# Kernel tuning notes

Measured on AMD Instinct MI355X. Metric: run time of the kernel, lower is better.

## Reference

```python
import jax, jax.numpy as jnp
import numpy as np

B, N, M, C, H = 8, 1024, 128, 1024, 16
D = C // H
MLP = int(C * 4.0)
EPS = 1e-6


def setup_inputs() -> dict:
    key = jax.random.key(0)
    ks = jax.random.split(key, 24)
    def w(k, shape):
        return jax.random.normal(k, shape, jnp.float32) * 0.02
    mask = jax.random.randint(ks[3], (B, M), 0, 2, dtype=jnp.int32)
    mask = mask.at[:, 0].set(1)  # ensure at least one attendable token per row
    return {
        "x": jax.random.normal(ks[0], (B, N, C), jnp.float32),
        "c_dino": jax.random.normal(ks[1], (B, C), jnp.float32),
        "c_text": jax.random.normal(ks[2], (B, M, C), jnp.float32),
        "text_mask": mask,
        "W_ada": w(ks[4], (C, 6 * C)), "b_ada": jnp.zeros((6 * C,), jnp.float32),
        "W_qkv": w(ks[5], (C, 3 * C)), "b_qkv": jnp.zeros((3 * C,), jnp.float32),
        "W_proj_sa": w(ks[6], (C, C)), "b_proj_sa": jnp.zeros((C,), jnp.float32),
        "W_q": w(ks[7], (C, C)), "b_q": jnp.zeros((C,), jnp.float32),
        "W_kv": w(ks[8], (C, 2 * C)), "b_kv": jnp.zeros((2 * C,), jnp.float32),
        "W_proj_ca": w(ks[9], (C, C)), "b_proj_ca": jnp.zeros((C,), jnp.float32),
        "W_fc1": w(ks[10], (C, MLP)), "b_fc1": jnp.zeros((MLP,), jnp.float32),
        "W_fc2": w(ks[11], (MLP, C)), "b_fc2": jnp.zeros((C,), jnp.float32),
    }


def _ln(x):
    # LayerNorm without affine params, eps=1e-6
    mu = jnp.mean(x, axis=-1, keepdims=True)
    xc = x - mu
    var = jnp.mean(xc * xc, axis=-1, keepdims=True)
    return xc * jax.lax.rsqrt(var + EPS)


def _modulate(x, shift, scale):
    return x * (1.0 + scale[:, None, :]) + shift[:, None, :]


def _heads(t):
    b, n, _ = t.shape
    return t.reshape(b, n, H, D)


def reference(x, c_dino, c_text, text_mask,
              W_ada, b_ada, W_qkv, b_qkv, W_proj_sa, b_proj_sa,
              W_q, b_q, W_kv, b_kv, W_proj_ca, b_proj_ca,
              W_fc1, b_fc1, W_fc2, b_fc2):
    scale = D ** (-0.5)
    ada = jax.nn.silu(c_dino) @ W_ada + b_ada  # (B, 6C)
    sh_msa, sc_msa, sh_ca, sc_ca, sh_mlp, sc_mlp = jnp.split(ada, 6, axis=1)

    # --- self-attention ---
    h = _modulate(_ln(x), sh_msa, sc_msa)
    qkv = h @ W_qkv + b_qkv
    q, k, v = (_heads(t) for t in jnp.split(qkv, 3, axis=-1))  # (B,N,H,D)
    attn = jax.nn.softmax(jnp.einsum('bnhd,bmhd->bhnm', q, k) * scale, axis=-1)
    sa = jnp.einsum('bhnm,bmhd->bnhd', attn, v).reshape(B, N, C) @ W_proj_sa + b_proj_sa
    x = x + sa

    # --- cross-attention ---
    h = _modulate(_ln(x), sh_ca, sc_ca)
    q = _heads(h @ W_q + b_q)                 # (B,N,H,D)
    kv = c_text @ W_kv + b_kv
    k, v = (_heads(t) for t in jnp.split(kv, 2, axis=-1))  # (B,M,H,D)
    scores = jnp.einsum('bnhd,bmhd->bhnm', q, k) * scale
    scores = jnp.where(text_mask[:, None, None, :] == 0, -jnp.inf, scores)
    attn = jax.nn.softmax(scores, axis=-1)
    ca = jnp.einsum('bhnm,bmhd->bnhd', attn, v).reshape(B, N, C) @ W_proj_ca + b_proj_ca
    x = x + ca

    # --- MLP ---
    h = _modulate(_ln(x), sh_mlp, sc_mlp)
    mlp = jax.nn.gelu(h @ W_fc1 + b_fc1, approximate=True) @ W_fc2 + b_fc2
    return x + mlp
```

## Files before the change

### kernel.cpp

```cpp
#include <hip/hip_runtime.h>
#include <hip/hip_bf16.h>

#define B_   8
#define N_   1024
#define M_   128
#define C_   1024
#define H_   16
#define D_   64
#define MLP_ 4096

typedef __bf16 bf16;
typedef __bf16 bf16x8 __attribute__((ext_vector_type(8)));
typedef __bf16 bf16x4 __attribute__((ext_vector_type(4)));
typedef float  f32x4  __attribute__((ext_vector_type(4)));

__device__ __forceinline__ f32x4 mfma16(bf16x8 a, bf16x8 b, f32x4 c) {
    return __builtin_amdgcn_mfma_f32_16x16x32_bf16(a, b, c, 0, 0, 0);
}

__device__ __forceinline__ void gload16(const bf16* g, bf16* l) {
    __builtin_amdgcn_global_load_lds(
        (const __attribute__((address_space(1))) void*)g,
        (__attribute__((address_space(3))) void*)l, 16, 0, 0);
}

__global__ __launch_bounds__(256) void transpose_k(const float* __restrict__ W,
                                                   bf16* __restrict__ Wt,
                                                   int K, int Nc) {
    __shared__ float tile[32][33];
    const int x  = threadIdx.x & 31;
    const int y0 = threadIdx.x >> 5;
    const size_t n0 = (size_t)blockIdx.x * 32;
    const size_t k0 = (size_t)blockIdx.y * 32;
#pragma unroll
    for (int i = 0; i < 4; i++)
        tile[y0 + i * 8][x] = W[(k0 + y0 + i * 8) * Nc + n0 + x];
    __syncthreads();
#pragma unroll
    for (int i = 0; i < 4; i++)
        Wt[(n0 + y0 + i * 8) * K + k0 + x] = (bf16)tile[x][y0 + i * 8];
}

__global__ __launch_bounds__(256) void vtrans_k(const bf16* __restrict__ in, int instride,
                                                int coff, int Mk, bf16* __restrict__ outT) {
    __shared__ bf16 t[32][33];
    const int tx = threadIdx.x & 31;
    const int ty0 = threadIdx.x >> 5;
    const int m0  = blockIdx.x * 32;
    const int hd0 = blockIdx.y * 32;
    const int b   = blockIdx.z;
#pragma unroll
    for (int i = 0; i < 4; i++)
        t[ty0 + i * 8][tx] = in[((size_t)(b * Mk + m0 + ty0 + i * 8)) * instride + coff + hd0 + tx];
    __syncthreads();
#pragma unroll
    for (int i = 0; i < 4; i++)
        outT[((size_t)(b * 1024 + hd0 + ty0 + i * 8)) * Mk + m0 + tx] = t[tx][ty0 + i * 8];
}

__global__ __launch_bounds__(256) void cvt_bf16_k(const float* __restrict__ in,
                                                  bf16* __restrict__ out, int n4) {
    int i = blockIdx.x * 256 + threadIdx.x;
    if (i < n4) {
        float4 v = ((const float4*)in)[i];
        bf16x4 o;
        o[0] = (bf16)v.x; o[1] = (bf16)v.y; o[2] = (bf16)v.z; o[3] = (bf16)v.w;
        ((bf16x4*)out)[i] = o;
    }
}

__global__ __launch_bounds__(256) void ada_init_k(const float* __restrict__ bias,
                                                  float* __restrict__ ada) {
    int i = blockIdx.x * 256 + threadIdx.x;
    ada[i] = bias[i % 6144];
}

__global__ __launch_bounds__(256) void ada_k(const float* __restrict__ cdino,
                                             const float* __restrict__ W,
                                             float* __restrict__ ada) {
    __shared__ float sc[8][32];
    const int tid = threadIdx.x;
    const int k0  = blockIdx.y * 32;
    {
        float c = cdino[(tid >> 5) * 1024 + k0 + (tid & 31)];
        sc[tid >> 5][tid & 31] = c / (1.f + __expf(-c));
    }
    __syncthreads();
    const int col = blockIdx.x * 256 + tid;
    float acc[8];
#pragma unroll
    for (int b = 0; b < 8; b++) acc[b] = 0.f;
    for (int kk = 0; kk < 32; kk++) {
        float w = W[(size_t)(k0 + kk) * 6144 + col];
#pragma unroll
        for (int b = 0; b < 8; b++) acc[b] += sc[b][kk] * w;
    }
#pragma unroll
    for (int b = 0; b < 8; b++) atomicAdd(&ada[(size_t)b * 6144 + col], acc[b]);
}

__global__ __launch_bounds__(256) void ln_mod_k(const float* __restrict__ X,
                                                const float* __restrict__ ada,
                                                int shoff, int scoff,
                                                bf16* __restrict__ Hout) {
    const int row = blockIdx.x;
    const int b   = row >> 10;
    const int tid = threadIdx.x;
    const float4 v = ((const float4*)(X + (size_t)row * C_))[tid];
    float s  = v.x + v.y + v.z + v.w;
    float sq = v.x * v.x + v.y * v.y + v.z * v.z + v.w * v.w;
#pragma unroll
    for (int off = 32; off; off >>= 1) {
        s  += __shfl_xor(s,  off);
        sq += __shfl_xor(sq, off);
    }
    __shared__ float rs_[4], rq_[4];
    if ((tid & 63) == 0) { rs_[tid >> 6] = s; rq_[tid >> 6] = sq; }
    __syncthreads();
    s  = rs_[0] + rs_[1] + rs_[2] + rs_[3];
    sq = rq_[0] + rq_[1] + rq_[2] + rq_[3];
    const float mu   = s * (1.f / 1024.f);
    const float var  = sq * (1.f / 1024.f) - mu * mu;
    const float rstd = rsqrtf(var + 1e-6f);
    const float4 scv = ((const float4*)(ada + (size_t)b * 6144 + scoff))[tid];
    const float4 shv = ((const float4*)(ada + (size_t)b * 6144 + shoff))[tid];
    bf16x4 o;
    o[0] = (bf16)(((v.x - mu) * rstd) * (1.f + scv.x) + shv.x);
    o[1] = (bf16)(((v.y - mu) * rstd) * (1.f + scv.y) + shv.y);
    o[2] = (bf16)(((v.z - mu) * rstd) * (1.f + scv.z) + shv.z);
    o[3] = (bf16)(((v.w - mu) * rstd) * (1.f + scv.w) + shv.w);
    *(bf16x4*)(Hout + (size_t)row * C_ + tid * 4) = o;
}

template <int MODE>
__global__ __launch_bounds__(512, 2) void gemm256w_k(const bf16* __restrict__ A,
                                                     const bf16* __restrict__ Bt,
                                                     const float* __restrict__ bias,
                                                     bf16* __restrict__ outB,
                                                     int Ncols, int K, int GX) {
    __shared__ __attribute__((aligned(16))) bf16 As[4][256][32];
    __shared__ __attribute__((aligned(16))) bf16 Bs[4][256][32];

    const int tid  = threadIdx.x;
    const int lane = tid & 63, wave = tid >> 6;
    const int lrow = lane & 15, quad = lane >> 4;
    const int wm = wave >> 2, wn = wave & 3;

    const unsigned lid = blockIdx.x;
    const unsigned cpx = gridDim.x >> 3;
    const unsigned g   = (lid & 7) * cpx + (lid >> 3);
    const size_t bm = (size_t)(g / GX) * 256;
    const size_t bn = (size_t)(g % GX) * 256;

    const int r0 = tid >> 2;
    const int cs = ((tid & 3) ^ ((r0 >> 1) & 3)) * 8;
    const bf16* gA0 = A  + (bm + r0) * (size_t)K + cs;
    const bf16* gA1 = gA0 + (size_t)128 * K;
    const bf16* gB0 = Bt + (bn + r0) * (size_t)K + cs;
    const bf16* gB1 = gB0 + (size_t)128 * K;

    f32x4 acc[8][4];
#pragma unroll
    for (int i = 0; i < 8; i++)
#pragma unroll
        for (int j = 0; j < 4; j++) acc[i][j] = (f32x4){0.f, 0.f, 0.f, 0.f};

    auto stage = [&](int bb, int koff) {
        bf16* la = &As[bb][0][0] + wave * 512;
        gload16(gA0 + koff, la);
        gload16(gA1 + koff, la + 4096);
        bf16* lb = &Bs[bb][0][0] + wave * 512;
        gload16(gB0 + koff, lb);
        gload16(gB1 + koff, lb + 4096);
    };

    const int xo = (quad ^ ((lrow >> 1) & 3)) * 8;

    bf16x8 bq[4], af[4];
    auto readB = [&](int bb) {
        const bf16(*Bp)[32] = Bs[bb];
#pragma unroll
        for (int ni = 0; ni < 4; ni++)
            bq[ni] = *(const bf16x8*)&Bp[wn * 64 + ni * 16 + lrow][xo];
    };
    auto readA4 = [&](int bb, int h) {
        const bf16(*Ap)[32] = As[bb];
#pragma unroll
        for (int mi = 0; mi < 4; mi++)
            af[mi] = *(const bf16x8*)&Ap[wm * 128 + h * 64 + mi * 16 + lrow][xo];
    };
    auto mfmac = [&](int h) {
        __builtin_amdgcn_s_setprio(1);
#pragma unroll
        for (int mi = 0; mi < 4; mi++)
#pragma unroll
            for (int ni = 0; ni < 4; ni++)
                acc[h * 4 + mi][ni] = mfma16(af[mi], bq[ni], acc[h * 4 + mi][ni]);
        __builtin_amdgcn_s_setprio(0);
    };

    auto step_body = [&](int c) {
        readB(c); readA4(c, 0);
        __builtin_amdgcn_s_barrier();
        mfmac(0);
        __builtin_amdgcn_s_barrier();
        readA4(c, 1);
        __builtin_amdgcn_s_barrier();
        mfmac(1);
    };

    stage(0, 0);
    stage(1, 32);
    stage(2, 64);
    asm volatile("s_waitcnt vmcnt(8)" ::: "memory");
    __builtin_amdgcn_s_barrier();

    const int KT = K >> 5;
    for (int s = 0; s < KT - 3; ++s) {
        const int c = s & 3;
        readB(c); readA4(c, 0);
        stage((s + 3) & 3, (s + 3) << 5);
        __builtin_amdgcn_s_barrier();
        mfmac(0);
        __builtin_amdgcn_s_barrier();
        readA4(c, 1);
        __builtin_amdgcn_s_barrier();
        mfmac(1);
        asm volatile("s_waitcnt vmcnt(8)" ::: "memory");
        __builtin_amdgcn_s_barrier();
    }
    {
        step_body((KT - 3) & 3);
        asm volatile("s_waitcnt vmcnt(4)" ::: "memory");
        __builtin_amdgcn_s_barrier();
    }
    {
        step_body((KT - 2) & 3);
        asm volatile("s_waitcnt vmcnt(0)" ::: "memory");
        __builtin_amdgcn_s_barrier();
    }
    {
        step_body((KT - 1) & 3);
    }

#pragma unroll
    for (int mi = 0; mi < 8; mi++) {
#pragma unroll
        for (int ni = 0; ni < 4; ni++) {
            const size_t gcol = bn + wn * 64 + ni * 16 + lrow;
            const float bv = bias[gcol];
#pragma unroll
            for (int r = 0; r < 4; r++) {
                const size_t grow = bm + wm * 128 + mi * 16 + quad * 4 + r;
                float v = acc[mi][ni][r] + bv;
                if (MODE == 3) {
                    float z = 1.59576912f * (v + 0.044715f * v * v * v);
                    v = v / (1.f + __expf(-z));
                }
                outB[grow * Ncols + gcol] = (bf16)v;
            }
        }
    }
}

template <int MODE>
__global__ __launch_bounds__(512, 2) void gemm256_k(const bf16* __restrict__ A,
                                                    const bf16* __restrict__ Bt,
                                                    const float* __restrict__ bias,
                                                    const float* resid,
                                                    float* outF, bf16* outB,
                                                    int Ncols, int K, int GX) {
    __shared__ __attribute__((aligned(16))) bf16 As[3][2][256][32];
    __shared__ __attribute__((aligned(16))) bf16 Bs[3][2][128][32];

    const int tid  = threadIdx.x;
    const int lane = tid & 63, wave = tid >> 6;
    const int lrow = lane & 15, quad = lane >> 4;
    const int wm = wave >> 2, wn = wave & 3;

    const unsigned lid = blockIdx.x;
    const unsigned cpx = gridDim.x >> 3;
    const unsigned g   = (lid & 7) * cpx + (lid >> 3);
    const size_t bm = (size_t)(g / GX) * 256;
    const size_t bn = (size_t)(g % GX) * 128;

    const int r0 = tid >> 2;
    const int cs = ((tid & 3) ^ ((r0 >> 1) & 3)) * 8;
    const bf16* gA0 = A  + (bm + r0) * (size_t)K + cs;
    const bf16* gA1 = gA0 + (size_t)128 * K;
    const bf16* gB0 = Bt + (bn + r0) * (size_t)K + cs;

    f32x4 acc[8][2];
#pragma unroll
    for (int i = 0; i < 8; i++)
#pragma unroll
        for (int j = 0; j < 2; j++) acc[i][j] = (f32x4){0.f, 0.f, 0.f, 0.f};

    auto stage = [&](int bb, int ks, int koff) {
        bf16* la = &As[bb][ks][0][0] + wave * 512;
        gload16(gA0 + koff, la);
        gload16(gA1 + koff, la + 4096);
        bf16* lb = &Bs[bb][ks][0][0] + wave * 512;
        gload16(gB0 + koff, lb);
    };

    const int xo = (quad ^ ((lrow >> 1) & 3)) * 8;

    bf16x8 bq[2], af[4];
    auto readB = [&](int bb, int ks) {
        const bf16(*Bp)[32] = Bs[bb][ks];
#pragma unroll
        for (int ni = 0; ni < 2; ni++)
            bq[ni] = *(const bf16x8*)&Bp[wn * 32 + ni * 16 + lrow][xo];
    };
    auto readA4 = [&](int bb, int ks, int h) {
        const bf16(*Ap)[32] = As[bb][ks];
#pragma unroll
        for (int mi = 0; mi < 4; mi++)
            af[mi] = *(const bf16x8*)&Ap[wm * 128 + h * 64 + mi * 16 + lrow][xo];
    };
    auto mfmac = [&](int h) {
        __builtin_amdgcn_s_setprio(1);
#pragma unroll
        for (int mi = 0; mi < 4; mi++)
#pragma unroll
            for (int ni = 0; ni < 2; ni++)
                acc[h * 4 + mi][ni] = mfma16(af[mi], bq[ni], acc[h * 4 + mi][ni]);
        __builtin_amdgcn_s_setprio(0);
    };

    stage(0, 0, 0);
    stage(0, 1, 32);
    stage(1, 0, 64);
    stage(1, 1, 96);
    asm volatile("s_waitcnt vmcnt(9)" ::: "memory");
    __builtin_amdgcn_s_barrier();

    const int KT = K >> 6;
    int c = 0, ct = 2;
    for (int kt = 0; kt < KT - 2; ++kt) {
        const int kn = (kt + 2) << 6;
        readB(c, 0); readA4(c, 0, 0);
        stage(ct, 0, kn);
        __builtin_amdgcn_s_barrier();
        mfmac(0);
        __builtin_amdgcn_s_barrier();
        readA4(c, 0, 1);
        __builtin_amdgcn_s_barrier();
        mfmac(1);
        asm volatile("s_waitcnt vmcnt(9)" ::: "memory");
        __builtin_amdgcn_s_barrier();
        readB(c, 1); readA4(c, 1, 0);
        stage(ct, 1, kn + 32);
        __builtin_amdgcn_s_barrier();
        mfmac(0);
        __builtin_amdgcn_s_barrier();
        readA4(c, 1, 1);
        __builtin_amdgcn_s_barrier();
        mfmac(1);
        asm volatile("s_waitcnt vmcnt(9)" ::: "memory");
        __builtin_amdgcn_s_barrier();
        c  = (c  == 2) ? 0 : c  + 1;
        ct = (ct == 2) ? 0 : ct + 1;
    }
    {
        readB(c, 0); readA4(c, 0, 0);
        __builtin_amdgcn_s_barrier();
        mfmac(0);
        __builtin_amdgcn_s_barrier();
        readA4(c, 0, 1);
        __builtin_amdgcn_s_barrier();
        mfmac(1);
        asm volatile("s_waitcnt vmcnt(6)" ::: "memory");
        __builtin_amdgcn_s_barrier();
        readB(c, 1); readA4(c, 1, 0);
        __builtin_amdgcn_s_barrier();
        mfmac(0);
        __builtin_amdgcn_s_barrier();
        readA4(c, 1, 1);
        __builtin_amdgcn_s_barrier();
        mfmac(1);
        asm volatile("s_waitcnt vmcnt(3)" ::: "memory");
        __builtin_amdgcn_s_barrier();
        c = (c == 2) ? 0 : c + 1;
    }
    {
        readB(c, 0); readA4(c, 0, 0);
        __builtin_amdgcn_s_barrier();
        mfmac(0);
        __builtin_amdgcn_s_barrier();
        readA4(c, 0, 1);
        __builtin_amdgcn_s_barrier();
        mfmac(1);
        asm volatile("s_waitcnt vmcnt(0)" ::: "memory");
        __builtin_amdgcn_s_barrier();
        readB(c, 1); readA4(c, 1, 0);
        __builtin_amdgcn_s_barrier();
        mfmac(0);
        __builtin_amdgcn_s_barrier();
        readA4(c, 1, 1);
        __builtin_amdgcn_s_barrier();
        mfmac(1);
    }

#pragma unroll
    for (int mi = 0; mi < 8; mi++) {
#pragma unroll
        for (int ni = 0; ni < 2; ni++) {
            const size_t gcol = bn + wn * 32 + ni * 16 + lrow;
            const float bv = bias[gcol];
#pragma unroll
            for (int r = 0; r < 4; r++) {
                const size_t grow = bm + wm * 128 + mi * 16 + quad * 4 + r;
                const size_t idx  = grow * Ncols + gcol;
                float v = acc[mi][ni][r] + bv;
                if (MODE == 1) {
                    outF[idx] = v + resid[idx];
                } else if (MODE == 2) {
                    outB[idx] = (bf16)v;
                } else {
                    float z = 1.59576912f * (v + 0.044715f * v * v * v);
                    outB[idx] = (bf16)(v / (1.f + __expf(-z)));
                }
            }
        }
    }
}

template <int MODE, int KS>
__global__ __launch_bounds__(256 * KS) void gemm_k(const bf16* __restrict__ A,
                                                   const bf16* __restrict__ Bt,
                                                   const float* __restrict__ bias,
                                                   const float* resid,
                                                   float* outF, bf16* outB,
                                                   int Ncols, int K, int GX) {
    __shared__ __attribute__((aligned(16))) bf16 As[2][KS][128][32];
    __shared__ __attribute__((aligned(16))) bf16 Bs[2][KS][128][32];
    const int tid  = threadIdx.x & 255;
    const int grp  = threadIdx.x >> 8;
    const int lane = tid & 63, wave = tid >> 6;
    const int lrow = lane & 15, quad = lane >> 4;
    const int wm = wave >> 1, wn = wave & 1;

    const unsigned lid = blockIdx.x;
    const unsigned xcd = lid & 7, s = lid >> 3;
    const unsigned bnb = s % GX, bmb = (s / GX) * 8 + xcd;
    const size_t bm = (size_t)bmb * 128;
    const size_t bn = (size_t)bnb * 128;

    const int Kh = K / KS;
    const int prow = tid >> 2, pseg = tid & 3;
    const int gseg = pseg ^ ((prow >> 1) & 3);
    const bf16* gA0 = A  + (bm + prow) * (size_t)K + grp * Kh + gseg * 8;
    const bf16* gA1 = gA0 + (size_t)64 * K;
    const bf16* gB0 = Bt + (bn + prow) * (size_t)K + grp * Kh + gseg * 8;
    const bf16* gB1 = gB0 + (size_t)64 * K;
    const int bufoff = KS * 128 * 32;
    bf16* lA = &As[0][grp][0][0] + wave * 512;
    bf16* lB = &Bs[0][grp][0][0] + wave * 512;

    const int xoff = (quad ^ ((lrow >> 1) & 3)) * 8;

    f32x4 acc[4][4];
#pragma unroll
    for (int i = 0; i < 4; i++)
#pragma unroll
        for (int j = 0; j < 4; j++) acc[i][j] = (f32x4){0.f, 0.f, 0.f, 0.f};

    {
        gload16(gA0, lA);
        gload16(gA1, lA + 2048);
        gload16(gB0, lB);
        gload16(gB1, lB + 2048);
    }
    int p = 0;
    for (int ko = 0; ko < Kh; ko += 32) {
        __syncthreads();
        if (ko + 32 < Kh) {
            const int po = (p ^ 1) * bufoff;
            gload16(gA0 + ko + 32, lA + po);
            gload16(gA1 + ko + 32, lA + po + 2048);
            gload16(gB0 + ko + 32, lB + po);
            gload16(gB1 + ko + 32, lB + po + 2048);
        }
        const bf16(*Asp)[32] = As[p][grp];
        const bf16(*Bsp)[32] = Bs[p][grp];
        bf16x8 af[4], bfr[4];
#pragma unroll
        for (int mi = 0; mi < 4; mi++)
            af[mi] = *(const bf16x8*)&Asp[wm * 64 + mi * 16 + lrow][xoff];
#pragma unroll
        for (int ni = 0; ni < 4; ni++)
            bfr[ni] = *(const bf16x8*)&Bsp[wn * 64 + ni * 16 + lrow][xoff];
#pragma unroll
        for (int mi = 0; mi < 4; mi++)
#pragma unroll
            for (int ni = 0; ni < 4; ni++)
                acc[mi][ni] = mfma16(af[mi], bfr[ni], acc[mi][ni]);
        p ^= 1;
    }

    if constexpr (KS == 2) {
        f32x4* red = (f32x4*)&As[0][0][0][0];
#pragma unroll
        for (int rnd = 0; rnd < 4; rnd++) {
            __syncthreads();
            if (grp == 1) {
#pragma unroll
                for (int c = 0; c < 4; c++) {
                    const int idx = rnd * 4 + c;
                    red[c * 256 + tid] = acc[idx >> 2][idx & 3];
                }
            }
            __syncthreads();
            if (grp == 0) {
#pragma unroll
                for (int c = 0; c < 4; c++) {
                    const int idx = rnd * 4 + c;
                    acc[idx >> 2][idx & 3] += red[c * 256 + tid];
                }
            }
        }
    }

    if (grp == 0) {
#pragma unroll
        for (int mi = 0; mi < 4; mi++) {
#pragma unroll
            for (int ni = 0; ni < 4; ni++) {
                const size_t gcol = bn + wn * 64 + ni * 16 + lrow;
                const float bv = bias[gcol];
#pragma unroll
                for (int r = 0; r < 4; r++) {
                    const size_t grow = bm + wm * 64 + mi * 16 + quad * 4 + r;
                    const size_t idx  = grow * Ncols + gcol;
                    float v = acc[mi][ni][r] + bv;
                    if (MODE == 1) {
                        outF[idx] = v + resid[idx];
                    } else if (MODE == 2) {
                        outB[idx] = (bf16)v;
                    } else {
                        float z = 1.59576912f * (v + 0.044715f * v * v * v);
                        outB[idx] = (bf16)(v / (1.f + __expf(-z)));
                    }
                }
            }
        }
    }
}

template <bool MASKED>
__global__ __launch_bounds__(256) void attn_k(const bf16* __restrict__ Qp, int qstride,
                                              const bf16* __restrict__ Kp, int kstride,
                                              const bf16* __restrict__ Vtg,
                                              const int* __restrict__ mask, int Mk,
                                              bf16* __restrict__ O) {
    __shared__ __attribute__((aligned(16))) bf16 Kt[64][88];
    __shared__ __attribute__((aligned(16))) bf16 Vt[64][88];
    __shared__ __attribute__((aligned(16))) bf16 Pt[4][16][88];
    __shared__ float madd[64];

    const int b = blockIdx.z, h = blockIdx.y;
    const int tid  = threadIdx.x;
    const int lane = tid & 63, wave = tid >> 6;
    const int lrow = lane & 15, quad = lane >> 4;
    const int q0 = blockIdx.x * 64 + wave * 16;

    const bf16* qp = Qp + ((size_t)(b * N_ + q0 + lrow)) * qstride + h * 64 + quad * 8;
    const bf16x8 bq0 = *(const bf16x8*)(qp);
    const bf16x8 bq1 = *(const bf16x8*)(qp + 32);

    f32x4 acc[4];
#pragma unroll
    for (int t = 0; t < 4; t++) acc[t] = (f32x4){0.f, 0.f, 0.f, 0.f};
    float mrun = -3e38f, lrun = 0.f;

    const int srow = tid >> 2;
    const int sseg = (tid & 3) * 16;

    const bf16* kbase = Kp + ((size_t)b * Mk + srow) * kstride + h * 64 + sseg;
    const bf16* vbase = Vtg + ((size_t)(b * 1024 + h * 64 + srow)) * Mk + sseg;

    for (int kc = 0; kc < Mk; kc += 64) {
        __syncthreads();
        const bf16* kp = kbase + (size_t)kc * kstride;
        bf16x8 k0 = *(const bf16x8*)kp;
        bf16x8 k1 = *(const bf16x8*)(kp + 8);
        *(bf16x8*)&Kt[srow][sseg]     = k0;
        *(bf16x8*)&Kt[srow][sseg + 8] = k1;
        const bf16* vp = vbase + kc;
        bf16x8 v0 = *(const bf16x8*)vp;
        bf16x8 v1 = *(const bf16x8*)(vp + 8);
        *(bf16x8*)&Vt[srow][sseg]     = v0;
        *(bf16x8*)&Vt[srow][sseg + 8] = v1;
        if (MASKED && tid < 64)
            madd[tid] = (mask[b * Mk + kc + tid] == 0) ? -1e30f : 0.f;
        __syncthreads();

        float sv[4][4];
#pragma unroll
        for (int t = 0; t < 4; t++) {
            f32x4 s = (f32x4){0.f, 0.f, 0.f, 0.f};
            bf16x8 ak0 = *(const bf16x8*)&Kt[t * 16 + lrow][quad * 8];
            s = mfma16(ak0, bq0, s);
            bf16x8 ak1 = *(const bf16x8*)&Kt[t * 16 + lrow][32 + quad * 8];
            s = mfma16(ak1, bq1, s);
#pragma unroll
            for (int r = 0; r < 4; r++) {
                float ma = MASKED ? madd[t * 16 + quad * 4 + r] : 0.f;
                sv[t][r] = s[r] * 0.125f + ma;
            }
        }

        float vmax = sv[0][0];
#pragma unroll
        for (int t = 0; t < 4; t++)
#pragma unroll
            for (int r = 0; r < 4; r++) vmax = fmaxf(vmax, sv[t][r]);
        vmax = fmaxf(vmax, __shfl_xor(vmax, 16));
        vmax = fmaxf(vmax, __shfl_xor(vmax, 32));
        const float mnew  = fmaxf(mrun, vmax);
        const float alpha = __expf(mrun - mnew);
        mrun = mnew;
        float rsum = 0.f;
#pragma unroll
        for (int t = 0; t < 4; t++) {
            bf16x4 p4;
#pragma unroll
            for (int r = 0; r < 4; r++) {
                float p = __expf(sv[t][r] - mnew);
                rsum += p;
                p4[r] = (bf16)p;
            }
            *(bf16x4*)&Pt[wave][lrow][t * 16 + quad * 4] = p4;
        }
        rsum += __shfl_xor(rsum, 16);
        rsum += __shfl_xor(rsum, 32);
        lrun = lrun * alpha + rsum;

        float alpha4[4];
#pragma unroll
        for (int r = 0; r < 4; r++) alpha4[r] = __shfl(alpha, quad * 4 + r);
#pragma unroll
        for (int t = 0; t < 4; t++)
#pragma unroll
            for (int r = 0; r < 4; r++) acc[t][r] *= alpha4[r];

        __syncthreads();
        const bf16x8 ap0 = *(const bf16x8*)&Pt[wave][lrow][quad * 8];
        const bf16x8 ap1 = *(const bf16x8*)&Pt[wave][lrow][32 + quad * 8];

#pragma unroll
        for (int t = 0; t < 4; t++) {
            bf16x8 bv0 = *(const bf16x8*)&Vt[t * 16 + lrow][quad * 8];
            acc[t] = mfma16(ap0, bv0, acc[t]);
            bf16x8 bv1 = *(const bf16x8*)&Vt[t * 16 + lrow][32 + quad * 8];
            acc[t] = mfma16(ap1, bv1, acc[t]);
        }
    }

    float linv = 1.f / lrun;
    float linv4[4];
#pragma unroll
    for (int r = 0; r < 4; r++) linv4[r] = __shfl(linv, quad * 4 + r);
#pragma unroll
    for (int r = 0; r < 4; r++) {
        const size_t grow = (size_t)(b * N_ + q0 + quad * 4 + r);
#pragma unroll
        for (int t = 0; t < 4; t++)
            O[grow * C_ + h * 64 + t * 16 + lrow] = (bf16)(acc[t][r] * linv4[r]);
    }
}

extern "C" void kernel_launch(void* const* d_in, const int* in_sizes, int n_in,
                              void* d_out, int out_size, void* d_ws, size_t ws_size,
                              hipStream_t stream) {
    const float* x     = (const float*)d_in[0];
    const float* cdino = (const float*)d_in[1];
    const float* ctext = (const float*)d_in[2];
    const int*   tmask = (const int*)d_in[3];
    const float* W_ada = (const float*)d_in[4];
    const float* b_ada = (const float*)d_in[5];
    const float* W_qkv = (const float*)d_in[6];
    const float* b_qkv = (const float*)d_in[7];
    const float* W_sa  = (const float*)d_in[8];
    const float* b_sa  = (const float*)d_in[9];
    const float* W_q   = (const float*)d_in[10];
    const float* b_q   = (const float*)d_in[11];
    const float* W_kv  = (const float*)d_in[12];
    const float* b_kv  = (const float*)d_in[13];
    const float* W_ca  = (const float*)d_in[14];
    const float* b_ca  = (const float*)d_in[15];
    const float* W_fc1 = (const float*)d_in[16];
    const float* b_fc1 = (const float*)d_in[17];
    const float* W_fc2 = (const float*)d_in[18];
    const float* b_fc2 = (const float*)d_in[19];
    float* out = (float*)d_out;

    char* ws = (char*)d_ws;
    size_t off = 0;
    auto alloc = [&](size_t bytes) -> char* {
        char* p = ws + off;
        off += (bytes + 255) & ~(size_t)255;
        return p;
    };
    float* ada  = (float*)alloc((size_t)8 * 6144 * 4);
    bf16* ctxb  = (bf16*)alloc((size_t)1024 * 1024 * 2);
    bf16* WqkvT = (bf16*)alloc((size_t)3072 * 1024 * 2);
    bf16* WsaT  = (bf16*)alloc((size_t)1024 * 1024 * 2);
    bf16* WqT   = (bf16*)alloc((size_t)1024 * 1024 * 2);
    bf16* WkvT  = (bf16*)alloc((size_t)2048 * 1024 * 2);
    bf16* WcaT  = (bf16*)alloc((size_t)1024 * 1024 * 2);
    bf16* Wfc1T = (bf16*)alloc((size_t)4096 * 1024 * 2);
    bf16* Wfc2T = (bf16*)alloc((size_t)1024 * 4096 * 2);
    float* xbuf = (float*)alloc((size_t)8192 * 1024 * 4);
    bf16* hbuf  = (bf16*)alloc((size_t)8192 * 1024 * 2);
    bf16* attnb = (bf16*)alloc((size_t)8192 * 1024 * 2);
    bf16* VtgSA = (bf16*)alloc((size_t)8192 * 1024 * 2);
    bf16* VtgCA = (bf16*)alloc((size_t)8192 * 128 * 2);
    bf16* pool  = (bf16*)alloc((size_t)8192 * 4096 * 2);
    if (off > ws_size) return;

    bf16* qkvb  = pool;
    bf16* qb    = pool;
    bf16* kvb   = pool + (size_t)8192 * 1024;
    bf16* gelub = pool;

    transpose_k<<<dim3(3072 / 32, 1024 / 32), 256, 0, stream>>>(W_qkv, WqkvT, 1024, 3072);
    transpose_k<<<dim3(1024 / 32, 1024 / 32), 256, 0, stream>>>(W_sa,  WsaT,  1024, 1024);
    transpose_k<<<dim3(1024 / 32, 1024 / 32), 256, 0, stream>>>(W_q,   WqT,   1024, 1024);
    transpose_k<<<dim3(2048 / 32, 1024 / 32), 256, 0, stream>>>(W_kv,  WkvT,  1024, 2048);
    transpose_k<<<dim3(1024 / 32, 1024 / 32), 256, 0, stream>>>(W_ca,  WcaT,  1024, 1024);
    transpose_k<<<dim3(4096 / 32, 1024 / 32), 256, 0, stream>>>(W_fc1, Wfc1T, 1024, 4096);
    transpose_k<<<dim3(1024 / 32, 4096 / 32), 256, 0, stream>>>(W_fc2, Wfc2T, 4096, 1024);
    cvt_bf16_k<<<1024, 256, 0, stream>>>(ctext, ctxb, 262144);

    ada_init_k<<<192, 256, 0, stream>>>(b_ada, ada);
    ada_k<<<dim3(24, 32), 256, 0, stream>>>(cdino, W_ada, ada);

    ln_mod_k<<<8192, 256, 0, stream>>>(x, ada, 0, 1024, hbuf);
    gemm256_k<2><<<32 * 24, 512, 0, stream>>>(hbuf, WqkvT, b_qkv, nullptr, nullptr, qkvb, 3072, 1024, 24);
    vtrans_k<<<dim3(32, 32, 8), 256, 0, stream>>>(qkvb, 3072, 2048, 1024, VtgSA);
    attn_k<false><<<dim3(16, 16, 8), 256, 0, stream>>>(qkvb, 3072, qkvb + 1024, 3072, VtgSA,
                                                       nullptr, 1024, attnb);
    gemm256_k<1><<<32 * 8, 512, 0, stream>>>(attnb, WsaT, b_sa, x, xbuf, nullptr, 1024, 1024, 8);

    ln_mod_k<<<8192, 256, 0, stream>>>(xbuf, ada, 2048, 3072, hbuf);
    gemm256_k<2><<<32 * 8, 512, 0, stream>>>(hbuf, WqT, b_q, nullptr, nullptr, qb, 1024, 1024, 8);
    gemm_k<2, 2><<<16 * 8, 512, 0, stream>>>(ctxb, WkvT, b_kv, nullptr, nullptr, kvb, 2048, 1024, 16);
    vtrans_k<<<dim3(4, 32, 8), 256, 0, stream>>>(kvb, 2048, 1024, 128, VtgCA);
    attn_k<true><<<dim3(16, 16, 8), 256, 0, stream>>>(qb, 1024, kvb, 2048, VtgCA,
                                                      tmask, 128, attnb);
    gemm256_k<1><<<32 * 8, 512, 0, stream>>>(attnb, WcaT, b_ca, xbuf, xbuf, nullptr, 1024, 1024, 8);

    ln_mod_k<<<8192, 256, 0, stream>>>(xbuf, ada, 4096, 5120, hbuf);
    gemm256w_k<3><<<32 * 16, 512, 0, stream>>>(hbuf, Wfc1T, b_fc1, gelub, 4096, 1024, 16);
    gemm256_k<1><<<32 * 8, 512, 0, stream>>>(gelub, Wfc2T, b_fc2, xbuf, out, nullptr, 1024, 4096, 8);
}
```

Measured before the change: 751.0 us.

## Replace 256x128 GEMM with intra-block split-K across two wave groups

After: 794.4 us. 5.8% more time.

```diff
diff --git a/kernel.cpp b/kernel.cpp
--- a/kernel.cpp
+++ b/kernel.cpp
@@ -133,6 +133,151 @@
 }
 
 template <int MODE>
+__global__ __launch_bounds__(512, 2) void gemm128s_k(const bf16* __restrict__ A,
+                                                     const bf16* __restrict__ Bt,
+                                                     const float* __restrict__ bias,
+                                                     const float* resid,
+                                                     float* outF, bf16* outB,
+                                                     int Ncols, int K, int GX) {
+    __shared__ __attribute__((aligned(16))) bf16 As[3][2][256][32];
+    __shared__ __attribute__((aligned(16))) bf16 Bs[3][2][128][32];
+
+    const int tid  = threadIdx.x;
+    const int lane = tid & 63, wave = tid >> 6;
+    const int grp  = wave >> 2, w4 = wave & 3;
+    const int wm = w4 >> 1, wn = w4 & 1;
+    const int lrow = lane & 15, quad = lane >> 4;
+
+    const unsigned lid = blockIdx.x;
+    const unsigned cpx = gridDim.x >> 3;
+    const unsigned g   = (lid & 7) * cpx + (lid >> 3);
+    const size_t bm = (size_t)(g / GX) * 256;
+    const size_t bn = (size_t)(g % GX) * 128;
+
+    const int Kh = K >> 1;
+    const size_t gK = (size_t)grp * Kh;
+
+    f32x4 acc[8][4];
+#pragma unroll
+    for (int i = 0; i < 8; i++)
+#pragma unroll
+        for (int j = 0; j < 4; j++) acc[i][j] = (f32x4){0.f, 0.f, 0.f, 0.f};
+
+    auto stage = [&](int bb, int koff) {
+        bf16* la = &As[bb][grp][0][0];
+#pragma unroll
+        for (int j = 0; j < 4; j++) {
+            const int chb = (w4 * 4 + j) * 64;
+            const int ch  = chb + lane;
+            const int row = ch >> 2;
+            const int cs  = ((ch & 3) ^ ((row >> 1) & 3)) * 8;
+            gload16(A + (bm + row) * (size_t)K + gK + koff + cs, la + chb * 8);
+        }
+        bf16* lb = &Bs[bb][grp][0][0];
+#pragma unroll
+        for (int j = 0; j < 2; j++) {
+            const int chb = (w4 * 2 + j) * 64;
+            const int ch  = chb + lane;
+            const int row = ch >> 2;
+            const int cs  = ((ch & 3) ^ ((row >> 1) & 3)) * 8;
+            gload16(Bt + (bn + row) * (size_t)K + gK + koff + cs, lb + chb * 8);
+        }
+    };
+
+    const int xo = (quad ^ ((lrow >> 1) & 3)) * 8;
+
+    bf16x8 bq[4], af[4];
+    auto readB = [&](int bb) {
+        const bf16(*Bp)[32] = Bs[bb][grp];
+#pragma unroll
+        for (int ni = 0; ni < 4; ni++)
+            bq[ni] = *(const bf16x8*)&Bp[wn * 64 + ni * 16 + lrow][xo];
+    };
+    auto readA4 = [&](int bb, int h) {
+        const bf16(*Ap)[32] = As[bb][grp];
+#pragma unroll
+        for (int mi = 0; mi < 4; mi++)
+            af[mi] = *(const bf16x8*)&Ap[wm * 128 + h * 64 + mi * 16 + lrow][xo];
+    };
+    auto mfmac = [&](int h) {
+        __builtin_amdgcn_s_setprio(1);
+#pragma unroll
+        for (int mi = 0; mi < 4; mi++)
+#pragma unroll
+            for (int ni = 0; ni < 4; ni++)
+                acc[h * 4 + mi][ni] = mfma16(af[mi], bq[ni], acc[h * 4 + mi][ni]);
+        __builtin_amdgcn_s_setprio(0);
+    };
+
+    stage(0, 0);
+    stage(1, 32);
+    asm volatile("s_waitcnt vmcnt(6)" ::: "memory");
+    __builtin_amdgcn_s_barrier();
+
+    const int KT = Kh >> 5;
+    for (int s = 0; s < KT; ++s) {
+        const int c = s % 3;
+        readB(c); readA4(c, 0);
+        if (s + 2 < KT) stage((s + 2) % 3, (s + 2) << 5);
+        __builtin_amdgcn_s_barrier();
+        mfmac(0);
+        __builtin_amdgcn_s_barrier();
+        readA4(c, 1);
+        __builtin_amdgcn_s_barrier();
+        mfmac(1);
+        if (s + 1 < KT) {
+            if (s + 2 < KT)
+                asm volatile("s_waitcnt vmcnt(6)" ::: "memory");
+            else
+                asm volatile("s_waitcnt vmcnt(0)" ::: "memory");
+            __builtin_amdgcn_s_barrier();
+        }
+    }
+
+    f32x4* red = (f32x4*)&As[0][0][0][0];
+#pragma unroll
+    for (int rnd = 0; rnd < 2; rnd++) {
+        __syncthreads();
+        if (grp == 1) {
+#pragma unroll
+            for (int j = 0; j < 16; j++)
+                red[j * 256 + w4 * 64 + lane] = acc[rnd * 4 + (j >> 2)][j & 3];
+        }
+        __syncthreads();
+        if (grp == 0) {
+#pragma unroll
+            for (int j = 0; j < 16; j++)
+                acc[rnd * 4 + (j >> 2)][j & 3] += red[j * 256 + w4 * 64 + lane];
+        }
+    }
+
+    if (grp == 0) {
+#pragma unroll
+        for (int mi = 0; mi < 8; mi++) {
+#pragma unroll
+            for (int ni = 0; ni < 4; ni++) {
+                const size_t gcol = bn + wn * 64 + ni * 16 + lrow;
+                const float bv = bias[gcol];
+#pragma unroll
+                for (int r = 0; r < 4; r++) {
+                    const size_t grow = bm + wm * 128 + mi * 16 + quad * 4 + r;
+                    const size_t idx  = grow * Ncols + gcol;
+                    float v = acc[mi][ni][r] + bv;
+                    if (MODE == 1) {
+                        outF[idx] = v + resid[idx];
+                    } else if (MODE == 2) {
+                        outB[idx] = (bf16)v;
+                    } else {
+                        float z = 1.59576912f * (v + 0.044715f * v * v * v);
+                        outB[idx] = (bf16)(v / (1.f + __expf(-z)));
+                    }
+                }
+            }
+        }
+    }
+}
+
+template <int MODE>
 __global__ __launch_bounds__(512, 2) void gemm256w_k(const bf16* __restrict__ A,
                                                      const bf16* __restrict__ Bt,
                                                      const float* __restrict__ bias,
@@ -258,170 +403,6 @@
                     v = v / (1.f + __expf(-z));
                 }
                 outB[grow * Ncols + gcol] = (bf16)v;
-            }
-        }
-    }
-}
-
-template <int MODE>
-__global__ __launch_bounds__(512, 2) void gemm256_k(const bf16* __restrict__ A,
-                                                    const bf16* __restrict__ Bt,
-                                                    const float* __restrict__ bias,
-                                                    const float* resid,
-                                                    float* outF, bf16* outB,
-                                                    int Ncols, int K, int GX) {
-    __shared__ __attribute__((aligned(16))) bf16 As[3][2][256][32];
-    __shared__ __attribute__((aligned(16))) bf16 Bs[3][2][128][32];
-
-    const int tid  = threadIdx.x;
-    const int lane = tid & 63, wave = tid >> 6;
-    const int lrow = lane & 15, quad = lane >> 4;
-    const int wm = wave >> 2, wn = wave & 3;
-
-    const unsigned lid = blockIdx.x;
-    const unsigned cpx = gridDim.x >> 3;
-    const unsigned g   = (lid & 7) * cpx + (lid >> 3);
-    const size_t bm = (size_t)(g / GX) * 256;
-    const size_t bn = (size_t)(g % GX) * 128;
-
-    const int r0 = tid >> 2;
-    const int cs = ((tid & 3) ^ ((r0 >> 1) & 3)) * 8;
-    const bf16* gA0 = A  + (bm + r0) * (size_t)K + cs;
-    const bf16* gA1 = gA0 + (size_t)128 * K;
-    const bf16* gB0 = Bt + (bn + r0) * (size_t)K + cs;
-
-    f32x4 acc[8][2];
-#pragma unroll
-    for (int i = 0; i < 8; i++)
-#pragma unroll
-        for (int j = 0; j < 2; j++) acc[i][j] = (f32x4){0.f, 0.f, 0.f, 0.f};
-
-    auto stage = [&](int bb, int ks, int koff) {
-        bf16* la = &As[bb][ks][0][0] + wave * 512;
-        gload16(gA0 + koff, la);
-        gload16(gA1 + koff, la + 4096);
-        bf16* lb = &Bs[bb][ks][0][0] + wave * 512;
-        gload16(gB0 + koff, lb);
-    };
-
-    const int xo = (quad ^ ((lrow >> 1) & 3)) * 8;
-
-    bf16x8 bq[2], af[4];
-    auto readB = [&](int bb, int ks) {
-        const bf16(*Bp)[32] = Bs[bb][ks];
-#pragma unroll
-        for (int ni = 0; ni < 2; ni++)
-            bq[ni] = *(const bf16x8*)&Bp[wn * 32 + ni * 16 + lrow][xo];
-    };
-    auto readA4 = [&](int bb, int ks, int h) {
-        const bf16(*Ap)[32] = As[bb][ks];
-#pragma unroll
-        for (int mi = 0; mi < 4; mi++)
-            af[mi] = *(const bf16x8*)&Ap[wm * 128 + h * 64 + mi * 16 + lrow][xo];
-    };
-    auto mfmac = [&](int h) {
-        __builtin_amdgcn_s_setprio(1);
-#pragma unroll
-        for (int mi = 0; mi < 4; mi++)
-#pragma unroll
-            for (int ni = 0; ni < 2; ni++)
-                acc[h * 4 + mi][ni] = mfma16(af[mi], bq[ni], acc[h * 4 + mi][ni]);
-        __builtin_amdgcn_s_setprio(0);
-    };
-
-    stage(0, 0, 0);
-    stage(0, 1, 32);
-    stage(1, 0, 64);
-    stage(1, 1, 96);
-    asm volatile("s_waitcnt vmcnt(9)" ::: "memory");
-    __builtin_amdgcn_s_barrier();
-
-    const int KT = K >> 6;
-    int c = 0, ct = 2;
-    for (int kt = 0; kt < KT - 2; ++kt) {
-        const int kn = (kt + 2) << 6;
-        readB(c, 0); readA4(c, 0, 0);
-        stage(ct, 0, kn);
-        __builtin_amdgcn_s_barrier();
-        mfmac(0);
-        __builtin_amdgcn_s_barrier();
-        readA4(c, 0, 1);
-        __builtin_amdgcn_s_barrier();
-        mfmac(1);
-        asm volatile("s_waitcnt vmcnt(9)" ::: "memory");
-        __builtin_amdgcn_s_barrier();
-        readB(c, 1); readA4(c, 1, 0);
-        stage(ct, 1, kn + 32);
-        __builtin_amdgcn_s_barrier();
-        mfmac(0);
-        __builtin_amdgcn_s_barrier();
-        readA4(c, 1, 1);
-        __builtin_amdgcn_s_barrier();
-        mfmac(1);
-        asm volatile("s_waitcnt vmcnt(9)" ::: "memory");
-        __builtin_amdgcn_s_barrier();
-        c  = (c  == 2) ? 0 : c  + 1;
-        ct = (ct == 2) ? 0 : ct + 1;
-    }
-    {
-        readB(c, 0); readA4(c, 0, 0);
-        __builtin_amdgcn_s_barrier();
-        mfmac(0);
-        __builtin_amdgcn_s_barrier();
-        readA4(c, 0, 1);
-        __builtin_amdgcn_s_barrier();
-        mfmac(1);
-        asm volatile("s_waitcnt vmcnt(6)" ::: "memory");
-        __builtin_amdgcn_s_barrier();
-        readB(c, 1); readA4(c, 1, 0);
-        __builtin_amdgcn_s_barrier();
-        mfmac(0);
-        __builtin_amdgcn_s_barrier();
-        readA4(c, 1, 1);
-        __builtin_amdgcn_s_barrier();
-        mfmac(1);
-        asm volatile("s_waitcnt vmcnt(3)" ::: "memory");
-        __builtin_amdgcn_s_barrier();
-        c = (c == 2) ? 0 : c + 1;
-    }
-    {
-        readB(c, 0); readA4(c, 0, 0);
-        __builtin_amdgcn_s_barrier();
-        mfmac(0);
-        __builtin_amdgcn_s_barrier();
-        readA4(c, 0, 1);
-        __builtin_amdgcn_s_barrier();
-        mfmac(1);
-        asm volatile("s_waitcnt vmcnt(0)" ::: "memory");
-        __builtin_amdgcn_s_barrier();
-        readB(c, 1); readA4(c, 1, 0);
-        __builtin_amdgcn_s_barrier();
-        mfmac(0);
-        __builtin_amdgcn_s_barrier();
-        readA4(c, 1, 1);
-        __builtin_amdgcn_s_barrier();
-        mfmac(1);
-    }
-
-#pragma unroll
-    for (int mi = 0; mi < 8; mi++) {
-#pragma unroll
-        for (int ni = 0; ni < 2; ni++) {
-            const size_t gcol = bn + wn * 32 + ni * 16 + lrow;
-            const float bv = bias[gcol];
-#pragma unroll
-            for (int r = 0; r < 4; r++) {
-                const size_t grow = bm + wm * 128 + mi * 16 + quad * 4 + r;
-                const size_t idx  = grow * Ncols + gcol;
-                float v = acc[mi][ni][r] + bv;
-                if (MODE == 1) {
-                    outF[idx] = v + resid[idx];
-                } else if (MODE == 2) {
-                    outB[idx] = (bf16)v;
-                } else {
-                    float z = 1.59576912f * (v + 0.044715f * v * v * v);
-                    outB[idx] = (bf16)(v / (1.f + __expf(-z)));
-                }
             }
         }
     }
@@ -739,21 +720,21 @@
     ada_k<<<dim3(24, 32), 256, 0, stream>>>(cdino, W_ada, ada);
 
     ln_mod_k<<<8192, 256, 0, stream>>>(x, ada, 0, 1024, hbuf);
-    gemm256_k<2><<<32 * 24, 512, 0, stream>>>(hbuf, WqkvT, b_qkv, nullptr, nullptr, qkvb, 3072, 1024, 24);
+    gemm128s_k<2><<<32 * 24, 512, 0, stream>>>(hbuf, WqkvT, b_qkv, nullptr, nullptr, qkvb, 3072, 1024, 24);
     vtrans_k<<<dim3(32, 32, 8), 256, 0, stream>>>(qkvb, 3072, 2048, 1024, VtgSA);
     attn_k<false><<<dim3(16, 16, 8), 256, 0, stream>>>(qkvb, 3072, qkvb + 1024, 3072, VtgSA,
                                                        nullptr, 1024, attnb);
-    gemm256_k<1><<<32 * 8, 512, 0, stream>>>(attnb, WsaT, b_sa, x, xbuf, nullptr, 1024, 1024, 8);
+    gemm128s_k<1><<<32 * 8, 512, 0, stream>>>(attnb, WsaT, b_sa, x, xbuf, nullptr, 1024, 1024, 8);
 
     ln_mod_k<<<8192, 256, 0, stream>>>(xbuf, ada, 2048, 3072, hbuf);
-    gemm256_k<2><<<32 * 8, 512, 0, stream>>>(hbuf, WqT, b_q, nullptr, nullptr, qb, 1024, 1024, 8);
+    gemm128s_k<2><<<32 * 8, 512, 0, stream>>>(hbuf, WqT, b_q, nullptr, nullptr, qb, 1024, 1024, 8);
     gemm_k<2, 2><<<16 * 8, 512, 0, stream>>>(ctxb, WkvT, b_kv, nullptr, nullptr, kvb, 2048, 1024, 16);
     vtrans_k<<<dim3(4, 32, 8), 256, 0, stream>>>(kvb, 2048, 1024, 128, VtgCA);
     attn_k<true><<<dim3(16, 16, 8), 256, 0, stream>>>(qb, 1024, kvb, 2048, VtgCA,
                                                       tmask, 128, attnb);
-    gemm256_k<1><<<32 * 8, 512, 0, stream>>>(attnb, WcaT, b_ca, xbuf, xbuf, nullptr, 1024, 1024, 8);
+    gemm128s_k<1><<<32 * 8, 512, 0, stream>>>(attnb, WcaT, b_ca, xbuf, xbuf, nullptr, 1024, 1024, 8);
 
     ln_mod_k<<<8192, 256, 0, stream>>>(xbuf, ada, 4096, 5120, hbuf);
     gemm256w_k<3><<<32 * 16, 512, 0, stream>>>(hbuf, Wfc1T, b_fc1, gelub, 4096, 1024, 16);
-    gemm256_k<1><<<32 * 8, 512, 0, stream>>>(gelub, Wfc2T, b_fc2, xbuf, out, nullptr, 1024, 4096, 8);
-}
+    gemm128s_k<1><<<32 * 8, 512, 0, stream>>>(gelub, Wfc2T, b_fc2, xbuf, out, nullptr, 1024, 4096, 8);
+}
```

## Use intra-block split-K GEMM kernel for fc2 projection

Applied to the files above, without the earlier changes.

After: 753.3 us. About the same (+0.3%).

```diff
diff --git a/kernel.cpp b/kernel.cpp
--- a/kernel.cpp
+++ b/kernel.cpp
@@ -258,6 +258,151 @@
                     v = v / (1.f + __expf(-z));
                 }
                 outB[grow * Ncols + gcol] = (bf16)v;
+            }
+        }
+    }
+}
+
+template <int MODE>
+__global__ __launch_bounds__(512, 2) void gemm128s_k(const bf16* __restrict__ A,
+                                                     const bf16* __restrict__ Bt,
+                                                     const float* __restrict__ bias,
+                                                     const float* resid,
+                                                     float* outF, bf16* outB,
+                                                     int Ncols, int K, int GX) {
+    __shared__ __attribute__((aligned(16))) bf16 As[3][2][256][32];
+    __shared__ __attribute__((aligned(16))) bf16 Bs[3][2][128][32];
+
+    const int tid  = threadIdx.x;
+    const int lane = tid & 63, wave = tid >> 6;
+    const int grp  = wave >> 2, w4 = wave & 3;
+    const int wm = w4 >> 1, wn = w4 & 1;
+    const int lrow = lane & 15, quad = lane >> 4;
+
+    const unsigned lid = blockIdx.x;
+    const unsigned cpx = gridDim.x >> 3;
+    const unsigned g   = (lid & 7) * cpx + (lid >> 3);
+    const size_t bm = (size_t)(g / GX) * 256;
+    const size_t bn = (size_t)(g % GX) * 128;
+
+    const int Kh = K >> 1;
+    const size_t gK = (size_t)grp * Kh;
+
+    f32x4 acc[8][4];
+#pragma unroll
+    for (int i = 0; i < 8; i++)
+#pragma unroll
+        for (int j = 0; j < 4; j++) acc[i][j] = (f32x4){0.f, 0.f, 0.f, 0.f};
+
+    auto stage = [&](int bb, int koff) {
+        bf16* la = &As[bb][grp][0][0];
+#pragma unroll
+        for (int j = 0; j < 4; j++) {
+            const int chb = (w4 * 4 + j) * 64;
+            const int ch  = chb + lane;
+            const int row = ch >> 2;
+            const int cs  = ((ch & 3) ^ ((row >> 1) & 3)) * 8;
+            gload16(A + (bm + row) * (size_t)K + gK + koff + cs, la + chb * 8);
+        }
+        bf16* lb = &Bs[bb][grp][0][0];
+#pragma unroll
+        for (int j = 0; j < 2; j++) {
+            const int chb = (w4 * 2 + j) * 64;
+            const int ch  = chb + lane;
+            const int row = ch >> 2;
+            const int cs  = ((ch & 3) ^ ((row >> 1) & 3)) * 8;
+            gload16(Bt + (bn + row) * (size_t)K + gK + koff + cs, lb + chb * 8);
+        }
+    };
+
+    const int xo = (quad ^ ((lrow >> 1) & 3)) * 8;
+
+    bf16x8 bq[4], af[4];
+    auto readB = [&](int bb) {
+        const bf16(*Bp)[32] = Bs[bb][grp];
+#pragma unroll
+        for (int ni = 0; ni < 4; ni++)
+            bq[ni] = *(const bf16x8*)&Bp[wn * 64 + ni * 16 + lrow][xo];
+    };
+    auto readA4 = [&](int bb, int h) {
+        const bf16(*Ap)[32] = As[bb][grp];
+#pragma unroll
+        for (int mi = 0; mi < 4; mi++)
+            af[mi] = *(const bf16x8*)&Ap[wm * 128 + h * 64 + mi * 16 + lrow][xo];
+    };
+    auto mfmac = [&](int h) {
+        __builtin_amdgcn_s_setprio(1);
+#pragma unroll
+        for (int mi = 0; mi < 4; mi++)
+#pragma unroll
+            for (int ni = 0; ni < 4; ni++)
+                acc[h * 4 + mi][ni] = mfma16(af[mi], bq[ni], acc[h * 4 + mi][ni]);
+        __builtin_amdgcn_s_setprio(0);
+    };
+
+    stage(0, 0);
+    stage(1, 32);
+    asm volatile("s_waitcnt vmcnt(6)" ::: "memory");
+    __builtin_amdgcn_s_barrier();
+
+    const int KT = Kh >> 5;
+    for (int s = 0; s < KT; ++s) {
+        const int c = s % 3;
+        readB(c); readA4(c, 0);
+        if (s + 2 < KT) stage((s + 2) % 3, (s + 2) << 5);
+        __builtin_amdgcn_s_barrier();
+        mfmac(0);
+        __builtin_amdgcn_s_barrier();
+        readA4(c, 1);
+        __builtin_amdgcn_s_barrier();
+        mfmac(1);
+        if (s + 1 < KT) {
+            if (s + 2 < KT)
+                asm volatile("s_waitcnt vmcnt(6)" ::: "memory");
+            else
+                asm volatile("s_waitcnt vmcnt(0)" ::: "memory");
+            __builtin_amdgcn_s_barrier();
+        }
+    }
+
+    f32x4* red = (f32x4*)&As[0][0][0][0];
+#pragma unroll
+    for (int rnd = 0; rnd < 2; rnd++) {
+        __syncthreads();
+        if (grp == 1) {
+#pragma unroll
+            for (int j = 0; j < 16; j++)
+                red[j * 256 + w4 * 64 + lane] = acc[rnd * 4 + (j >> 2)][j & 3];
+        }
+        __syncthreads();
+        if (grp == 0) {
+#pragma unroll
+            for (int j = 0; j < 16; j++)
+                acc[rnd * 4 + (j >> 2)][j & 3] += red[j * 256 + w4 * 64 + lane];
+        }
+    }
+
+    if (grp == 0) {
+#pragma unroll
+        for (int mi = 0; mi < 8; mi++) {
+#pragma unroll
+            for (int ni = 0; ni < 4; ni++) {
+                const size_t gcol = bn + wn * 64 + ni * 16 + lrow;
+                const float bv = bias[gcol];
+#pragma unroll
+                for (int r = 0; r < 4; r++) {
+                    const size_t grow = bm + wm * 128 + mi * 16 + quad * 4 + r;
+                    const size_t idx  = grow * Ncols + gcol;
+                    float v = acc[mi][ni][r] + bv;
+                    if (MODE == 1) {
+                        outF[idx] = v + resid[idx];
+                    } else if (MODE == 2) {
+                        outB[idx] = (bf16)v;
+                    } else {
+                        float z = 1.59576912f * (v + 0.044715f * v * v * v);
+                        outB[idx] = (bf16)(v / (1.f + __expf(-z)));
+                    }
+                }
             }
         }
     }
@@ -755,5 +900,5 @@
 
     ln_mod_k<<<8192, 256, 0, stream>>>(xbuf, ada, 4096, 5120, hbuf);
     gemm256w_k<3><<<32 * 16, 512, 0, stream>>>(hbuf, Wfc1T, b_fc1, gelub, 4096, 1024, 16);
-    gemm256_k<1><<<32 * 8, 512, 0, stream>>>(gelub, Wfc2T, b_fc2, xbuf, out, nullptr, 1024, 4096, 8);
-}
+    gemm128s_k<1><<<32 * 8, 512, 0, stream>>>(gelub, Wfc2T, b_fc2, xbuf, out, nullptr, 1024, 4096, 8);
+}
```
